# Kernel optimization log

Hardware: AMD Instinct MI355X
Metric: run time of the kernel (lower is better)

## Reference

```python
import jax, jax.numpy as jnp
import numpy as np

B = 1024
D = 768          # 2 * hidden_size
HID = 384        # hidden_size (split point for mu/sigma)
MLP_H = 300      # InfoNCE hidden size
LOG2PI = float(np.log(2.0 * np.pi))


def setup_inputs() -> dict:
    key = jax.random.key(0)
    ks = jax.random.split(key, 12)
    s = 0.02
    return {
        "zl": jax.random.normal(ks[0], (B, 20, D), jnp.float32),
        "zv": jax.random.normal(ks[1], (B, 36, D), jnp.float32),
        "fc_l_w": jax.random.normal(ks[2], (20,), jnp.float32) * s,
        "fc_l_b": jax.random.normal(ks[3], (), jnp.float32) * s,
        "fc_v_w": jax.random.normal(ks[4], (36,), jnp.float32) * s,
        "fc_v_b": jax.random.normal(ks[5], (), jnp.float32) * s,
        "W1": jax.random.normal(ks[6], (MLP_H, 2 * HID), jnp.float32) * s,
        "b1": jnp.zeros((MLP_H,), jnp.float32),
        "W2": jax.random.normal(ks[7], (1, MLP_H), jnp.float32) * s,
        "b2": jnp.zeros((1,), jnp.float32),
        "eps1": jax.random.normal(ks[8], (B, HID), jnp.float32),
        "eps2": jax.random.normal(ks[9], (B, HID), jnp.float32),
        "perm": jax.random.permutation(ks[10], B),
    }


def _log_prob(mu, sigma, x):
    # Independent(Normal(mu, sigma), 1).log_prob(x)
    z = (x - mu) / sigma
    return jnp.sum(-jnp.log(sigma) - 0.5 * LOG2PI - 0.5 * z * z, axis=-1)


def reference(zl, zv, fc_l_w, fc_l_b, fc_v_w, fc_v_b, W1, b1, W2, b2, eps1, eps2, perm):
    # fc over token dim: permute(0,2,1) @ Linear(20->1) -> [B, D]
    z1 = jnp.einsum('bsd,s->bd', zl, fc_l_w) + fc_l_b
    z2 = jnp.einsum('bsd,s->bd', zv, fc_v_w) + fc_v_b

    mu1, sig1 = z1[:, :HID], jax.nn.softplus(z1[:, HID:]) + 1e-7
    mu2, sig2 = z2[:, :HID], jax.nn.softplus(z2[:, HID:]) + 1e-7

    # rsample
    s1 = mu1 + sig1 * eps1  # [B, HID]
    s2 = mu2 + sig2 * eps2

    kl_1_2 = _log_prob(mu1, sig1, s1) - _log_prob(mu2, sig2, s1)
    kl_2_1 = _log_prob(mu2, sig2, s2) - _log_prob(mu1, sig1, s2)
    d_skl = jnp.mean(kl_1_2 + kl_2_1) / 2.0

    # InfoNCE(x=s1, y=s2): F(x,y) = softplus(relu([x,y]W1^T + b1) W2^T + b2)
    W1x, W1y = W1[:, :HID], W1[:, HID:]
    Ax = s1 @ W1x.T            # [B, MLP_H], x contribution
    By = s2 @ W1y.T            # [B, MLP_H], y contribution
    w2 = W2[0]                 # [MLP_H]

    # T0: matched pairs
    T0 = jax.nn.softplus(jax.nn.relu(Ax + By + b1) @ w2 + b2[0])  # [B]

    # T1[i, j] = F(x_j, y_perm[i]); tile via broadcasting instead of repeat+cat
    By_p = By[perm]                                             # [B, MLP_H]
    h = jax.nn.relu(Ax[None, :, :] + By_p[:, None, :] + b1)     # [B, B, MLP_H]
    T1 = jax.nn.softplus(h @ w2 + b2[0])                        # [B, B]

    lower_bound = T0.mean() - (jax.scipy.special.logsumexp(T1, axis=1).mean() - jnp.log(jnp.float32(B)))
    return d_skl - lower_bound
```

## Files before the change

### kernel.cpp

```cpp
#include <hip/hip_runtime.h>
#include <math.h>

#define BB   1024
#define DD   768
#define HIDV 384
#define MLPH 300
#define MLPP 320

__device__ __forceinline__ float softplusf(float x) {
    return (x > 20.f) ? x : log1pf(expf(x));
}

__device__ __forceinline__ void f4arr(float4 v, float* o) {
    o[0] = v.x; o[1] = v.y; o[2] = v.z; o[3] = v.w;
}

__global__ void k_init(float* __restrict__ ws) {
    int i = blockIdx.x * 256 + threadIdx.x;
    if (i < 16 + BB) ws[i] = 0.f;
}

__global__ __launch_bounds__(192, 3) void k_rs(
    const float* __restrict__ zl, const float* __restrict__ zv,
    const float* __restrict__ wl, const float* __restrict__ blp,
    const float* __restrict__ wv, const float* __restrict__ bvp,
    const float* __restrict__ eps1, const float* __restrict__ eps2,
    float* __restrict__ s1, float* __restrict__ s2, float* __restrict__ accum)
{
    int b = blockIdx.x;
    int t = threadIdx.x;
    const float4* zl4 = (const float4*)zl + b * (20 * 192) + t;
    const float4* zv4 = (const float4*)zv + b * (36 * 192) + t;

    float z1v[4] = {0,0,0,0}, z2v[4] = {0,0,0,0};
    #pragma unroll
    for (int s = 0; s < 20; ++s) {
        float w = wl[s];
        float a[4];
        f4arr(zl4[s * 192], a);
        #pragma unroll
        for (int j = 0; j < 4; ++j) z1v[j] = fmaf(a[j], w, z1v[j]);
    }
    #pragma unroll
    for (int s = 0; s < 36; ++s) {
        float w = wv[s];
        float a[4];
        f4arr(zv4[s * 192], a);
        #pragma unroll
        for (int j = 0; j < 4; ++j) z2v[j] = fmaf(a[j], w, z2v[j]);
    }

    float bl = blp[0], bv = bvp[0];

    __shared__ __align__(16) float sg1s[HIDV];
    __shared__ __align__(16) float sg2s[HIDV];

    if (t >= 96) {
        float o1[4], o2[4];
        #pragma unroll
        for (int j = 0; j < 4; ++j) {
            o1[j] = softplusf(z1v[j] + bl) + 1e-7f;
            o2[j] = softplusf(z2v[j] + bv) + 1e-7f;
        }
        ((float4*)sg1s)[t - 96] = make_float4(o1[0], o1[1], o1[2], o1[3]);
        ((float4*)sg2s)[t - 96] = make_float4(o2[0], o2[1], o2[2], o2[3]);
    }
    __syncthreads();

    float con = 0.f;
    if (t < 96) {
        float e1v[4], e2v[4], g1[4], g2[4];
        f4arr(((const float4*)eps1)[b * 96 + t], e1v);
        f4arr(((const float4*)eps2)[b * 96 + t], e2v);
        f4arr(((const float4*)sg1s)[t], g1);
        f4arr(((const float4*)sg2s)[t], g2);
        float s1o[4], s2o[4];
        #pragma unroll
        for (int j = 0; j < 4; ++j) {
            float mu1 = z1v[j] + bl;
            float mu2 = z2v[j] + bv;
            float sg1 = g1[j], sg2 = g2[j];
            float e1 = e1v[j], e2 = e2v[j];
            float sv1 = fmaf(sg1, e1, mu1);
            float sv2 = fmaf(sg2, e2, mu2);
            s1o[j] = sv1; s2o[j] = sv2;
            float z12 = (sv1 - mu2) / sg2;
            float z21 = (sv2 - mu1) / sg1;
            con += -0.5f * (e1 * e1 + e2 * e2) + 0.5f * z12 * z12 + 0.5f * z21 * z21;
        }
        ((float4*)s1)[b * 96 + t] = make_float4(s1o[0], s1o[1], s1o[2], s1o[3]);
        ((float4*)s2)[b * 96 + t] = make_float4(s2o[0], s2o[1], s2o[2], s2o[3]);
    }

    #pragma unroll
    for (int m = 1; m < 64; m <<= 1) con += __shfl_xor(con, m);
    __shared__ float pr[3];
    if ((t & 63) == 0) pr[t >> 6] = con;
    __syncthreads();
    if (t == 0) atomicAdd(&accum[0], pr[0] + pr[1] + pr[2]);
}

__global__ __launch_bounds__(256) void k_gemm(
    const float* __restrict__ s1, const float* __restrict__ s2,
    const float* __restrict__ W1, const float* __restrict__ b1,
    float* __restrict__ Axb, float* __restrict__ By)
{
    __shared__ __align__(16) float Ss[32][68];
    __shared__ __align__(16) float Ws[32][68];
    int z = blockIdx.z;
    const float* S = z ? s2 : s1;
    float* Out = z ? By : Axb;
    int wofs = z ? HIDV : 0;
    int b0 = blockIdx.x * 64;
    int k0 = blockIdx.y * 64;
    int tid = threadIdx.x;
    int r = tid >> 2;
    int c4 = tid & 3;
    int tx = tid & 15, ty = tid >> 4;

    float4 ps[2], pw[2];
    int krow = k0 + r;
    auto ld = [&](int hc) {
        #pragma unroll
        for (int u = 0; u < 2; ++u) {
            int hq = (c4 + 4 * u) * 4;
            ps[u] = *(const float4*)&S[(b0 + r) * HIDV + hc + hq];
            pw[u] = (krow < MLPH) ? *(const float4*)&W1[krow * DD + wofs + hc + hq]
                                  : make_float4(0.f, 0.f, 0.f, 0.f);
        }
    };
    ld(0);
    float acc[4][4] = {{0.f}};
    for (int ch = 0; ch < 12; ++ch) {
        __syncthreads();
        #pragma unroll
        for (int u = 0; u < 2; ++u) {
            int hq = (c4 + 4 * u) * 4;
            Ss[hq + 0][r] = ps[u].x; Ss[hq + 1][r] = ps[u].y;
            Ss[hq + 2][r] = ps[u].z; Ss[hq + 3][r] = ps[u].w;
            Ws[hq + 0][r] = pw[u].x; Ws[hq + 1][r] = pw[u].y;
            Ws[hq + 2][r] = pw[u].z; Ws[hq + 3][r] = pw[u].w;
        }
        __syncthreads();
        if (ch < 11) ld((ch + 1) * 32);
        #pragma unroll
        for (int h = 0; h < 32; ++h) {
            float sv[4], wv4[4];
            f4arr(*(const float4*)&Ss[h][ty * 4], sv);
            f4arr(*(const float4*)&Ws[h][tx * 4], wv4);
            #pragma unroll
            for (int i = 0; i < 4; ++i)
                #pragma unroll
                for (int j = 0; j < 4; ++j)
                    acc[i][j] = fmaf(sv[i], wv4[j], acc[i][j]);
        }
    }
    #pragma unroll
    for (int i = 0; i < 4; ++i) {
        int bb = b0 + ty * 4 + i;
        float o[4];
        #pragma unroll
        for (int j = 0; j < 4; ++j) {
            int k = k0 + tx * 4 + j;
            float v = acc[i][j];
            if (!z) v += b1[k < MLPH ? k : 0];
            o[j] = (k < MLPH) ? v : 0.f;
        }
        *(float4*)&Out[bb * MLPP + k0 + tx * 4] = make_float4(o[0], o[1], o[2], o[3]);
    }
}

__global__ void k_t0(const float* __restrict__ Axb, const float* __restrict__ By,
                     const float* __restrict__ W2, const float* __restrict__ b2,
                     float* __restrict__ accum)
{
    int b = blockIdx.x;
    int l = threadIdx.x;
    float t = 0.f;
    for (int k = l; k < MLPH; k += 64)
        t = fmaf(fmaxf(Axb[b * MLPP + k] + By[b * MLPP + k], 0.f), W2[k], t);
    #pragma unroll
    for (int m = 1; m < 64; m <<= 1) t += __shfl_xor(t, m);
    if (l == 0) atomicAdd(&accum[1], softplusf(t + b2[0]));
}

__global__ __launch_bounds__(256) void k_pairs(
    const float* __restrict__ Axb, const float* __restrict__ By,
    const int* __restrict__ perm, const float* __restrict__ W2,
    const float* __restrict__ b2, float* __restrict__ sumexp)
{
    __shared__ __align__(16) float As[64][68];
    __shared__ __align__(16) float Bs[64][68];
    __shared__ float w2s[MLPP];
    int tid = threadIdx.x;
    int j0 = blockIdx.x * 64;
    int i0 = blockIdx.y * 64;
    for (int t = tid; t < MLPP; t += 256) w2s[t] = (t < MLPH) ? W2[t] : 0.f;
    int r = tid >> 2;
    int c4 = tid & 3;
    int tx = tid & 15, ty = tid >> 4;
    int prow = perm[i0 + r];

    float4 pa[4], pb[4];
    auto ld = [&](int kc) {
        #pragma unroll
        for (int u = 0; u < 4; ++u) {
            int kq = (c4 + 4 * u) * 4;
            pa[u] = *(const float4*)&Axb[(j0 + r) * MLPP + kc + kq];
            pb[u] = *(const float4*)&By[prow * MLPP + kc + kq];
        }
    };
    ld(0);
    float acc[4][4] = {{0.f}};
    for (int ch = 0; ch < 5; ++ch) {
        __syncthreads();
        #pragma unroll
        for (int u = 0; u < 4; ++u) {
            int kq = (c4 + 4 * u) * 4;
            As[kq + 0][r] = pa[u].x; As[kq + 1][r] = pa[u].y;
            As[kq + 2][r] = pa[u].z; As[kq + 3][r] = pa[u].w;
            Bs[kq + 0][r] = pb[u].x; Bs[kq + 1][r] = pb[u].y;
            Bs[kq + 2][r] = pb[u].z; Bs[kq + 3][r] = pb[u].w;
        }
        __syncthreads();
        if (ch < 4) ld((ch + 1) * 64);
        int kc = ch * 64;
        #pragma unroll
        for (int k = 0; k < 64; ++k) {
            float w = w2s[kc + k];
            float avv[4], bvv[4];
            f4arr(*(const float4*)&As[k][tx * 4], avv);
            f4arr(*(const float4*)&Bs[k][ty * 4], bvv);
            #pragma unroll
            for (int c = 0; c < 4; ++c)
                #pragma unroll
                for (int d = 0; d < 4; ++d)
                    acc[c][d] = fmaf(fmaxf(avv[d] + bvv[c], 0.f), w, acc[c][d]);
        }
    }
    float b2v = b2[0];
    #pragma unroll
    for (int c = 0; c < 4; ++c) {
        float ssum = 0.f;
        #pragma unroll
        for (int d = 0; d < 4; ++d) {
            ssum += 1.f + expf(acc[c][d] + b2v);
        }
        ssum += __shfl_xor(ssum, 1);
        ssum += __shfl_xor(ssum, 2);
        ssum += __shfl_xor(ssum, 4);
        ssum += __shfl_xor(ssum, 8);
        if (tx == 0) atomicAdd(&sumexp[i0 + ty * 4 + c], ssum);
    }
}

__global__ __launch_bounds__(256) void k_final(
    const float* __restrict__ accum, const float* __restrict__ sumexp,
    float* __restrict__ out)
{
    int tid = threadIdx.x;
    float s = 0.f;
    for (int i = tid; i < BB; i += 256) s += logf(sumexp[i]);
    #pragma unroll
    for (int m = 1; m < 64; m <<= 1) s += __shfl_xor(s, m);
    __shared__ float red[4];
    if ((tid & 63) == 0) red[tid >> 6] = s;
    __syncthreads();
    if (tid == 0) {
        float lse_mean = (red[0] + red[1] + red[2] + red[3]) / (float)BB;
        float d_skl = accum[0] / (2.f * (float)BB);
        float t0_mean = accum[1] / (float)BB;
        float lower = t0_mean - (lse_mean - logf((float)BB));
        out[0] = d_skl - lower;
    }
}

extern "C" void kernel_launch(void* const* d_in, const int* in_sizes, int n_in,
                              void* d_out, int out_size, void* d_ws, size_t ws_size,
                              hipStream_t stream)
{
    const float* zl     = (const float*)d_in[0];
    const float* zv     = (const float*)d_in[1];
    const float* fc_l_w = (const float*)d_in[2];
    const float* fc_l_b = (const float*)d_in[3];
    const float* fc_v_w = (const float*)d_in[4];
    const float* fc_v_b = (const float*)d_in[5];
    const float* W1     = (const float*)d_in[6];
    const float* b1     = (const float*)d_in[7];
    const float* W2     = (const float*)d_in[8];
    const float* b2     = (const float*)d_in[9];
    const float* eps1   = (const float*)d_in[10];
    const float* eps2   = (const float*)d_in[11];
    const int*   perm   = (const int*)d_in[12];
    float* out = (float*)d_out;

    float* ws     = (float*)d_ws;
    float* accum  = ws;
    float* sumexp = ws + 16;
    float* s1     = ws + 16 + BB;
    float* s2     = s1 + BB * HIDV;
    float* Axb    = s2 + BB * HIDV;
    float* By     = Axb + BB * MLPP;

    k_init<<<5, 256, 0, stream>>>(ws);
    k_rs<<<BB, 192, 0, stream>>>(zl, zv, fc_l_w, fc_l_b, fc_v_w, fc_v_b,
                                 eps1, eps2, s1, s2, accum);
    k_gemm<<<dim3(16, 5, 2), 256, 0, stream>>>(s1, s2, W1, b1, Axb, By);
    k_t0<<<BB, 64, 0, stream>>>(Axb, By, W2, b2, accum);
    k_pairs<<<dim3(16, 16), 256, 0, stream>>>(Axb, By, perm, W2, b2, sumexp);
    k_final<<<1, 256, 0, stream>>>(accum, sumexp, out);
}
```

Before: 313.9 us.

## Use packed float2 math in pair and GEMM kernels, batch two rows per reduce block

The pairwise relu-MLP kernel and the small GEMM now use two-wide float vectors with elementwise fma and max, so the compiler can emit packed FP32 instructions and roughly halve the VALU instruction count in the hot loops. The GEMM tile shrinks to 32 rows per block, doubling its grid. The token-reduction kernel handles two batch rows per block to expose more memory-level parallelism. The packed ops depend on codegen actually producing packed instructions, and the extra accumulators could raise register pressure.

```diff
diff --git a/kernel.cpp b/kernel.cpp
--- a/kernel.cpp
+++ b/kernel.cpp
@@ -7,6 +7,8 @@
 #define MLPH 300
 #define MLPP 320
 
+typedef float v2f __attribute__((ext_vector_type(2)));
+
 __device__ __forceinline__ float softplusf(float x) {
     return (x > 20.f) ? x : log1pf(expf(x));
 }
@@ -20,76 +22,102 @@
     if (i < 16 + BB) ws[i] = 0.f;
 }
 
-__global__ __launch_bounds__(192, 3) void k_rs(
+__global__ __launch_bounds__(192, 4) void k_rs(
     const float* __restrict__ zl, const float* __restrict__ zv,
     const float* __restrict__ wl, const float* __restrict__ blp,
     const float* __restrict__ wv, const float* __restrict__ bvp,
     const float* __restrict__ eps1, const float* __restrict__ eps2,
     float* __restrict__ s1, float* __restrict__ s2, float* __restrict__ accum)
 {
-    int b = blockIdx.x;
+    int b0 = blockIdx.x * 2;
     int t = threadIdx.x;
-    const float4* zl4 = (const float4*)zl + b * (20 * 192) + t;
-    const float4* zv4 = (const float4*)zv + b * (36 * 192) + t;
-
-    float z1v[4] = {0,0,0,0}, z2v[4] = {0,0,0,0};
+    const float4* zlA = (const float4*)zl + b0 * (20 * 192) + t;
+    const float4* zlB = zlA + 20 * 192;
+    const float4* zvA = (const float4*)zv + b0 * (36 * 192) + t;
+    const float4* zvB = zvA + 36 * 192;
+
+    float z1a[4] = {0,0,0,0}, z1b[4] = {0,0,0,0};
+    float z2a[4] = {0,0,0,0}, z2b[4] = {0,0,0,0};
+
     #pragma unroll
     for (int s = 0; s < 20; ++s) {
         float w = wl[s];
-        float a[4];
-        f4arr(zl4[s * 192], a);
-        #pragma unroll
-        for (int j = 0; j < 4; ++j) z1v[j] = fmaf(a[j], w, z1v[j]);
+        float a[4], c[4];
+        f4arr(zlA[s * 192], a);
+        f4arr(zlB[s * 192], c);
+        #pragma unroll
+        for (int j = 0; j < 4; ++j) {
+            z1a[j] = fmaf(a[j], w, z1a[j]);
+            z1b[j] = fmaf(c[j], w, z1b[j]);
+        }
     }
     #pragma unroll
     for (int s = 0; s < 36; ++s) {
         float w = wv[s];
-        float a[4];
-        f4arr(zv4[s * 192], a);
-        #pragma unroll
-        for (int j = 0; j < 4; ++j) z2v[j] = fmaf(a[j], w, z2v[j]);
+        float a[4], c[4];
+        f4arr(zvA[s * 192], a);
+        f4arr(zvB[s * 192], c);
+        #pragma unroll
+        for (int j = 0; j < 4; ++j) {
+            z2a[j] = fmaf(a[j], w, z2a[j]);
+            z2b[j] = fmaf(c[j], w, z2b[j]);
+        }
     }
 
     float bl = blp[0], bv = bvp[0];
 
-    __shared__ __align__(16) float sg1s[HIDV];
-    __shared__ __align__(16) float sg2s[HIDV];
+    __shared__ __align__(16) float sg1s[2][HIDV];
+    __shared__ __align__(16) float sg2s[2][HIDV];
 
     if (t >= 96) {
+        int u = t - 96;
         float o1[4], o2[4];
         #pragma unroll
         for (int j = 0; j < 4; ++j) {
-            o1[j] = softplusf(z1v[j] + bl) + 1e-7f;
-            o2[j] = softplusf(z2v[j] + bv) + 1e-7f;
-        }
-        ((float4*)sg1s)[t - 96] = make_float4(o1[0], o1[1], o1[2], o1[3]);
-        ((float4*)sg2s)[t - 96] = make_float4(o2[0], o2[1], o2[2], o2[3]);
+            o1[j] = softplusf(z1a[j] + bl) + 1e-7f;
+            o2[j] = softplusf(z2a[j] + bv) + 1e-7f;
+        }
+        ((float4*)sg1s[0])[u] = make_float4(o1[0], o1[1], o1[2], o1[3]);
+        ((float4*)sg2s[0])[u] = make_float4(o2[0], o2[1], o2[2], o2[3]);
+        #pragma unroll
+        for (int j = 0; j < 4; ++j) {
+            o1[j] = softplusf(z1b[j] + bl) + 1e-7f;
+            o2[j] = softplusf(z2b[j] + bv) + 1e-7f;
+        }
+        ((float4*)sg1s[1])[u] = make_float4(o1[0], o1[1], o1[2], o1[3]);
+        ((float4*)sg2s[1])[u] = make_float4(o2[0], o2[1], o2[2], o2[3]);
     }
     __syncthreads();
 
     float con = 0.f;
     if (t < 96) {
-        float e1v[4], e2v[4], g1[4], g2[4];
-        f4arr(((const float4*)eps1)[b * 96 + t], e1v);
-        f4arr(((const float4*)eps2)[b * 96 + t], e2v);
-        f4arr(((const float4*)sg1s)[t], g1);
-        f4arr(((const float4*)sg2s)[t], g2);
-        float s1o[4], s2o[4];
-        #pragma unroll
-        for (int j = 0; j < 4; ++j) {
-            float mu1 = z1v[j] + bl;
-            float mu2 = z2v[j] + bv;
-            float sg1 = g1[j], sg2 = g2[j];
-            float e1 = e1v[j], e2 = e2v[j];
-            float sv1 = fmaf(sg1, e1, mu1);
-            float sv2 = fmaf(sg2, e2, mu2);
-            s1o[j] = sv1; s2o[j] = sv2;
-            float z12 = (sv1 - mu2) / sg2;
-            float z21 = (sv2 - mu1) / sg1;
-            con += -0.5f * (e1 * e1 + e2 * e2) + 0.5f * z12 * z12 + 0.5f * z21 * z21;
-        }
-        ((float4*)s1)[b * 96 + t] = make_float4(s1o[0], s1o[1], s1o[2], s1o[3]);
-        ((float4*)s2)[b * 96 + t] = make_float4(s2o[0], s2o[1], s2o[2], s2o[3]);
+        #pragma unroll
+        for (int rr = 0; rr < 2; ++rr) {
+            int b = b0 + rr;
+            const float* zm1 = rr ? z1b : z1a;
+            const float* zm2 = rr ? z2b : z2a;
+            float e1v[4], e2v[4], g1[4], g2[4];
+            f4arr(((const float4*)eps1)[b * 96 + t], e1v);
+            f4arr(((const float4*)eps2)[b * 96 + t], e2v);
+            f4arr(((const float4*)sg1s[rr])[t], g1);
+            f4arr(((const float4*)sg2s[rr])[t], g2);
+            float s1o[4], s2o[4];
+            #pragma unroll
+            for (int j = 0; j < 4; ++j) {
+                float mu1 = zm1[j] + bl;
+                float mu2 = zm2[j] + bv;
+                float sg1 = g1[j], sg2 = g2[j];
+                float e1 = e1v[j], e2 = e2v[j];
+                float sv1 = fmaf(sg1, e1, mu1);
+                float sv2 = fmaf(sg2, e2, mu2);
+                s1o[j] = sv1; s2o[j] = sv2;
+                float z12 = (sv1 - mu2) / sg2;
+                float z21 = (sv2 - mu1) / sg1;
+                con += -0.5f * (e1 * e1 + e2 * e2) + 0.5f * z12 * z12 + 0.5f * z21 * z21;
+            }
+            ((float4*)s1)[b * 96 + t] = make_float4(s1o[0], s1o[1], s1o[2], s1o[3]);
+            ((float4*)s2)[b * 96 + t] = make_float4(s2o[0], s2o[1], s2o[2], s2o[3]);
+        }
     }
 
     #pragma unroll
@@ -105,64 +133,68 @@
     const float* __restrict__ W1, const float* __restrict__ b1,
     float* __restrict__ Axb, float* __restrict__ By)
 {
-    __shared__ __align__(16) float Ss[32][68];
+    __shared__ __align__(16) float Ss[32][36];
     __shared__ __align__(16) float Ws[32][68];
     int z = blockIdx.z;
     const float* S = z ? s2 : s1;
     float* Out = z ? By : Axb;
     int wofs = z ? HIDV : 0;
-    int b0 = blockIdx.x * 64;
+    int b0 = blockIdx.x * 32;
     int k0 = blockIdx.y * 64;
     int tid = threadIdx.x;
-    int r = tid >> 2;
-    int c4 = tid & 3;
+    int srow = tid >> 3, sc = tid & 7;
+    int wrow = tid >> 2, wc = tid & 3;
+    int krow = k0 + wrow;
     int tx = tid & 15, ty = tid >> 4;
 
-    float4 ps[2], pw[2];
-    int krow = k0 + r;
+    float4 ps, pw[2];
     auto ld = [&](int hc) {
-        #pragma unroll
-        for (int u = 0; u < 2; ++u) {
-            int hq = (c4 + 4 * u) * 4;
-            ps[u] = *(const float4*)&S[(b0 + r) * HIDV + hc + hq];
-            pw[u] = (krow < MLPH) ? *(const float4*)&W1[krow * DD + wofs + hc + hq]
+        ps = *(const float4*)&S[(b0 + srow) * HIDV + hc + sc * 4];
+        #pragma unroll
+        for (int u = 0; u < 2; ++u)
+            pw[u] = (krow < MLPH) ? *(const float4*)&W1[krow * DD + wofs + hc + wc * 4 + u * 16]
                                   : make_float4(0.f, 0.f, 0.f, 0.f);
-        }
     };
     ld(0);
-    float acc[4][4] = {{0.f}};
+    v2f acc[2][2];
+    acc[0][0] = (v2f){0.f, 0.f}; acc[0][1] = (v2f){0.f, 0.f};
+    acc[1][0] = (v2f){0.f, 0.f}; acc[1][1] = (v2f){0.f, 0.f};
+
     for (int ch = 0; ch < 12; ++ch) {
         __syncthreads();
+        Ss[sc * 4 + 0][srow] = ps.x; Ss[sc * 4 + 1][srow] = ps.y;
+        Ss[sc * 4 + 2][srow] = ps.z; Ss[sc * 4 + 3][srow] = ps.w;
         #pragma unroll
         for (int u = 0; u < 2; ++u) {
-            int hq = (c4 + 4 * u) * 4;
-            Ss[hq + 0][r] = ps[u].x; Ss[hq + 1][r] = ps[u].y;
-            Ss[hq + 2][r] = ps[u].z; Ss[hq + 3][r] = ps[u].w;
-            Ws[hq + 0][r] = pw[u].x; Ws[hq + 1][r] = pw[u].y;
-            Ws[hq + 2][r] = pw[u].z; Ws[hq + 3][r] = pw[u].w;
+            int hb = wc * 4 + u * 16;
+            Ws[hb + 0][wrow] = pw[u].x; Ws[hb + 1][wrow] = pw[u].y;
+            Ws[hb + 2][wrow] = pw[u].z; Ws[hb + 3][wrow] = pw[u].w;
         }
         __syncthreads();
         if (ch < 11) ld((ch + 1) * 32);
         #pragma unroll
         for (int h = 0; h < 32; ++h) {
-            float sv[4], wv4[4];
-            f4arr(*(const float4*)&Ss[h][ty * 4], sv);
-            f4arr(*(const float4*)&Ws[h][tx * 4], wv4);
-            #pragma unroll
-            for (int i = 0; i < 4; ++i)
-                #pragma unroll
-                for (int j = 0; j < 4; ++j)
-                    acc[i][j] = fmaf(sv[i], wv4[j], acc[i][j]);
-        }
-    }
-    #pragma unroll
-    for (int i = 0; i < 4; ++i) {
-        int bb = b0 + ty * 4 + i;
+            v2f sv = *(const v2f*)&Ss[h][ty * 2];
+            float4 wq = *(const float4*)&Ws[h][tx * 4];
+            v2f w0 = (v2f){wq.x, wq.y};
+            v2f w1 = (v2f){wq.z, wq.w};
+            v2f s0 = (v2f){sv.x, sv.x};
+            v2f s1b = (v2f){sv.y, sv.y};
+            acc[0][0] = __builtin_elementwise_fma(s0, w0, acc[0][0]);
+            acc[0][1] = __builtin_elementwise_fma(s0, w1, acc[0][1]);
+            acc[1][0] = __builtin_elementwise_fma(s1b, w0, acc[1][0]);
+            acc[1][1] = __builtin_elementwise_fma(s1b, w1, acc[1][1]);
+        }
+    }
+    #pragma unroll
+    for (int i = 0; i < 2; ++i) {
+        int bb = b0 + ty * 2 + i;
+        float vraw[4] = {acc[i][0].x, acc[i][0].y, acc[i][1].x, acc[i][1].y};
         float o[4];
         #pragma unroll
         for (int j = 0; j < 4; ++j) {
             int k = k0 + tx * 4 + j;
-            float v = acc[i][j];
+            float v = vraw[j];
             if (!z) v += b1[k < MLPH ? k : 0];
             o[j] = (k < MLPH) ? v : 0.f;
         }
@@ -211,7 +243,12 @@
         }
     };
     ld(0);
-    float acc[4][4] = {{0.f}};
+    v2f acc2[4][2];
+    #pragma unroll
+    for (int c = 0; c < 4; ++c) {
+        acc2[c][0] = (v2f){0.f, 0.f};
+        acc2[c][1] = (v2f){0.f, 0.f};
+    }
     for (int ch = 0; ch < 5; ++ch) {
         __syncthreads();
         #pragma unroll
@@ -228,24 +265,31 @@
         #pragma unroll
         for (int k = 0; k < 64; ++k) {
             float w = w2s[kc + k];
-            float avv[4], bvv[4];
-            f4arr(*(const float4*)&As[k][tx * 4], avv);
-            f4arr(*(const float4*)&Bs[k][ty * 4], bvv);
+            v2f wv2 = (v2f){w, w};
+            float4 af = *(const float4*)&As[k][tx * 4];
+            float4 bf = *(const float4*)&Bs[k][ty * 4];
+            v2f a2[2] = { (v2f){af.x, af.y}, (v2f){af.z, af.w} };
+            float bs[4] = {bf.x, bf.y, bf.z, bf.w};
             #pragma unroll
-            for (int c = 0; c < 4; ++c)
+            for (int c = 0; c < 4; ++c) {
+                v2f bc = (v2f){bs[c], bs[c]};
                 #pragma unroll
-                for (int d = 0; d < 4; ++d)
-                    acc[c][d] = fmaf(fmaxf(avv[d] + bvv[c], 0.f), w, acc[c][d]);
+                for (int d2 = 0; d2 < 2; ++d2) {
+                    v2f tv = a2[d2] + bc;
+                    tv = __builtin_elementwise_max(tv, (v2f){0.f, 0.f});
+                    acc2[c][d2] = __builtin_elementwise_fma(tv, wv2, acc2[c][d2]);
+                }
+            }
         }
     }
     float b2v = b2[0];
     #pragma unroll
     for (int c = 0; c < 4; ++c) {
+        float vv[4] = {acc2[c][0].x, acc2[c][0].y, acc2[c][1].x, acc2[c][1].y};
         float ssum = 0.f;
         #pragma unroll
-        for (int d = 0; d < 4; ++d) {
-            ssum += 1.f + expf(acc[c][d] + b2v);
-        }
+        for (int d = 0; d < 4; ++d)
+            ssum += 1.f + expf(vv[d] + b2v);
         ssum += __shfl_xor(ssum, 1);
         ssum += __shfl_xor(ssum, 2);
         ssum += __shfl_xor(ssum, 4);
@@ -303,9 +347,9 @@
     float* By     = Axb + BB * MLPP;
 
     k_init<<<5, 256, 0, stream>>>(ws);
-    k_rs<<<BB, 192, 0, stream>>>(zl, zv, fc_l_w, fc_l_b, fc_v_w, fc_v_b,
-                                 eps1, eps2, s1, s2, accum);
-    k_gemm<<<dim3(16, 5, 2), 256, 0, stream>>>(s1, s2, W1, b1, Axb, By);
+    k_rs<<<BB / 2, 192, 0, stream>>>(zl, zv, fc_l_w, fc_l_b, fc_v_w, fc_v_b,
+                                     eps1, eps2, s1, s2, accum);
+    k_gemm<<<dim3(32, 5, 2), 256, 0, stream>>>(s1, s2, W1, b1, Axb, By);
     k_t0<<<BB, 64, 0, stream>>>(Axb, By, W2, b2, accum);
     k_pairs<<<dim3(16, 16), 256, 0, stream>>>(Axb, By, perm, W2, b2, sumexp);
     k_final<<<1, 256, 0, stream>>>(accum, sumexp, out);
```

Result: no change. 314.7 us (+0.3%).
